# Optimization experiments

Hardware: AMD Instinct MI355X
Metric: run time of the kernel (lower is better)

Reference implementation:

```python
import jax, jax.numpy as jnp
import numpy as np

B, T, D, H, N = 16, 512, 256, 4, 10
DK = D // H
EPS = 1e-12  # espnet LayerNorm eps


def _pe(t, d):
    # espnet PositionalEncoding table
    pos = np.arange(t, dtype=np.float32)[:, None]
    div = np.exp(np.arange(0, d, 2, dtype=np.float32) * (-np.log(10000.0) / d))
    pe = np.zeros((t, d), dtype=np.float32)
    pe[:, 0::2] = np.sin(pos * div)
    pe[:, 1::2] = np.cos(pos * div)
    return jnp.asarray(pe)


def _ln(x, g, b):
    m = jnp.mean(x, -1, keepdims=True)
    v = jnp.var(x, -1, keepdims=True)
    return (x - m) * jax.lax.rsqrt(v + EPS) * g + b


def _forward(x, x_lengths, lids, Wq, bq, Wk, bk, Wv, bv, Wo, bo, W1, b1, W2, b2, g1, be1, g2, be2, gf, bef):
    b, t, d = x.shape
    pe = _pe(t, d)
    pad = jnp.arange(t)[None, :] < x_lengths[:, None]          # [b,t] non-pad mask
    amask = pad[:, None, None, :]                               # [b,1,1,t] key mask
    onehot = (lids[:, None] == jnp.arange(N)[None, :]).astype(x.dtype)  # [b,N]
    h0 = x * np.float32(np.sqrt(d)) + pe[None]                  # scaled input + pos-enc (shared across experts)
    neg = jnp.finfo(x.dtype).min
    out = jnp.zeros_like(x)
    for z in range(N):  # fixed small set of structurally-distinct experts
        # pre-norm self-attention block
        hn = _ln(h0, g1[z], be1[z])
        q = (hn @ Wq[z] + bq[z]).reshape(b, t, H, DK).transpose(0, 2, 1, 3)
        k_ = (hn @ Wk[z] + bk[z]).reshape(b, t, H, DK).transpose(0, 2, 1, 3)
        v_ = (hn @ Wv[z] + bv[z]).reshape(b, t, H, DK).transpose(0, 2, 1, 3)
        scores = jnp.einsum('bhqd,bhkd->bhqk', q, k_) / np.float32(np.sqrt(DK))
        attn = jax.nn.softmax(jnp.where(amask, scores, neg), axis=-1)
        attn = jnp.where(amask, attn, jnp.zeros((), x.dtype))
        ctx = jnp.einsum('bhqk,bhkd->bhqd', attn, v_).transpose(0, 2, 1, 3).reshape(b, t, d)
        h = h0 + ctx @ Wo[z] + bo[z]
        # pre-norm feed-forward block
        hn2 = _ln(h, g2[z], be2[z])
        h = h + jax.nn.relu(hn2 @ W1[z] + b1[z]) @ W2[z] + b2[z]
        # final after_norm, then one-hot masked combine (== emb_lang sum)
        out = out + onehot[:, z, None, None] * _ln(h, gf[z], bef[z])
    return out


def setup_inputs() -> dict:
    key = jax.random.key(0)
    ks = jax.random.split(key, 12)
    s = np.float32(0.02)
    FF = 4 * D
    return {
        'x': jax.random.normal(ks[0], (B, T, D), jnp.float32),
        'x_lengths': jax.random.randint(ks[1], (B,), T // 2, T + 1),
        'lids': jax.random.randint(ks[2], (B,), 0, N),
        'Wq': jax.random.normal(ks[3], (N, D, D), jnp.float32) * s,
        'bq': jnp.zeros((N, D), jnp.float32),
        'Wk': jax.random.normal(ks[4], (N, D, D), jnp.float32) * s,
        'bk': jnp.zeros((N, D), jnp.float32),
        'Wv': jax.random.normal(ks[5], (N, D, D), jnp.float32) * s,
        'bv': jnp.zeros((N, D), jnp.float32),
        'Wo': jax.random.normal(ks[6], (N, D, D), jnp.float32) * s,
        'bo': jnp.zeros((N, D), jnp.float32),
        'W1': jax.random.normal(ks[7], (N, D, FF), jnp.float32) * s,
        'b1': jnp.zeros((N, FF), jnp.float32),
        'W2': jax.random.normal(ks[8], (N, FF, D), jnp.float32) * s,
        'b2': jnp.zeros((N, D), jnp.float32),
        'g1': jnp.ones((N, D), jnp.float32),
        'be1': jnp.zeros((N, D), jnp.float32),
        'g2': jnp.ones((N, D), jnp.float32),
        'be2': jnp.zeros((N, D), jnp.float32),
        'gf': jnp.ones((N, D), jnp.float32),
        'bef': jnp.zeros((N, D), jnp.float32),
    }


def reference(x, x_lengths, lids, Wq, bq, Wk, bk, Wv, bv, Wo, bo, W1, b1, W2, b2, g1, be1, g2, be2, gf, bef):
    return _forward(x, x_lengths, lids, Wq, bq, Wk, bk, Wv, bv, Wo, bo, W1, b1, W2, b2, g1, be1, g2, be2, gf, bef)
```

## Files before the change

kernel.cpp:

```cpp
#include <hip/hip_runtime.h>

typedef unsigned short u16;
typedef __bf16 bf16x8 __attribute__((ext_vector_type(8)));
typedef float  f32x4  __attribute__((ext_vector_type(4)));
typedef unsigned int   u32x4 __attribute__((ext_vector_type(4)));
typedef unsigned short u16x4 __attribute__((ext_vector_type(4)));

#define DEV __device__ __forceinline__

#define NB   16
#define TT   512
#define DD   256
#define HH   4
#define DKH  64
#define NLANG 10
#define FFD  1024

DEV u16 f2bf(float f) {
  unsigned int u = __builtin_bit_cast(unsigned int, f);
  return (u16)((u + 0x7fffu + ((u >> 16) & 1u)) >> 16);
}

DEV float bf2f(u16 u) {
  unsigned int x = ((unsigned int)u) << 16;
  return __builtin_bit_cast(float, x);
}

DEV f32x4 zero4() { f32x4 z; z[0]=0.f; z[1]=0.f; z[2]=0.f; z[3]=0.f; return z; }

typedef __attribute__((address_space(1))) const unsigned int g_as1;
typedef __attribute__((address_space(3))) unsigned int l_as3;
DEV void load_lds16(const void* g, void* l) {
  __builtin_amdgcn_global_load_lds((g_as1*)g, (l_as3*)l, 16, 0, 0);
}

DEV bf16x8 lds_frag(const u16* lds, int row, int slot) {
  return *(const bf16x8*)(lds + row * 64 + ((slot ^ (row & 7)) << 3));
}

__global__ __launch_bounds__(256) void pre_kernel(
    const float* __restrict__ Wq, const float* __restrict__ Wk,
    const float* __restrict__ Wv, const float* __restrict__ Wo,
    const float* __restrict__ W1, const float* __restrict__ W2,
    u16* __restrict__ wtq, u16* __restrict__ wtk, u16* __restrict__ wtv,
    u16* __restrict__ wto, u16* __restrict__ wt1, u16* __restrict__ wt2,
    const float* __restrict__ x, u16* __restrict__ h0, u16* __restrict__ hn,
    const float* __restrict__ g, const float* __restrict__ be,
    const int* __restrict__ lids) {
  __shared__ u16 tile[64][33];
  const int bx = blockIdx.x;
  if (bx < 3840) {
    const float* src; u16* dst; int R, C, z, r0, c0;
    if (bx < 1280) {
      const int w = bx / 320, rem = bx % 320;
      src = (w == 0) ? Wq : (w == 1) ? Wk : (w == 2) ? Wv : Wo;
      dst = (w == 0) ? wtq : (w == 1) ? wtk : (w == 2) ? wtv : wto;
      R = 256; C = 256; z = rem >> 5;
      const int rc = rem & 31; r0 = (rc >> 3) * 64; c0 = (rc & 7) * 32;
    } else if (bx < 2560) {
      const int rem = bx - 1280; src = W1; dst = wt1; R = 256; C = 1024;
      z = rem >> 7; const int rc = rem & 127; r0 = (rc >> 5) * 64; c0 = (rc & 31) * 32;
    } else {
      const int rem = bx - 2560; src = W2; dst = wt2; R = 1024; C = 256;
      z = rem >> 7; const int rc = rem & 127; r0 = (rc >> 3) * 64; c0 = (rc & 7) * 32;
    }
    bool used = false;
#pragma unroll
    for (int i = 0; i < NB; ++i) used |= (lids[i] == z);
    if (!used) return;
    const float* s = src + (size_t)z * R * C;
    u16* d = dst + (size_t)z * R * C;
    const int tx = threadIdx.x & 31, ty = threadIdx.x >> 5;
#pragma unroll
    for (int rr = 0; rr < 8; ++rr) {
      const int r = ty + rr * 8;
      tile[r][tx] = f2bf(s[(size_t)(r0 + r) * C + c0 + tx]);
    }
    __syncthreads();
#pragma unroll
    for (int rr = 0; rr < 4; ++rr) {
      const int cc = ty + rr * 8;
      const unsigned int lo = tile[tx * 2][cc], hi = tile[tx * 2 + 1][cc];
      *(unsigned int*)(d + (size_t)(c0 + cc) * R + r0 + tx * 2) = lo | (hi << 16);
    }
  } else {
    const int wave = threadIdx.x >> 6, lane = threadIdx.x & 63;
    const int row = (bx - 3840) * 4 + wave;
    const int b = row >> 9, t = row & 511;
    const int z = lids[b];
    const int c0 = lane * 4;
    const float4 xv = *(const float4*)(x + (size_t)row * DD + c0);
    const float kPE = -9.21034037197618f / 256.0f;
    float div0 = __expf(kPE * (float)c0);
    float div1 = __expf(kPE * (float)(c0 + 2));
    float a0 = div0 * (float)t, a1 = div1 * (float)t;
    float h[4];
    h[0] = xv.x * 16.0f + sinf(a0);
    h[1] = xv.y * 16.0f + cosf(a0);
    h[2] = xv.z * 16.0f + sinf(a1);
    h[3] = xv.w * 16.0f + cosf(a1);
    float s = h[0] + h[1] + h[2] + h[3];
    float ss = h[0]*h[0] + h[1]*h[1] + h[2]*h[2] + h[3]*h[3];
#pragma unroll
    for (int d = 1; d < 64; d <<= 1) { s += __shfl_xor(s, d); ss += __shfl_xor(ss, d); }
    float mean = s * (1.0f / 256.0f);
    float var  = ss * (1.0f / 256.0f) - mean * mean;
    float rstd = rsqrtf(var + 1e-12f);
    u16x4 h0v;
#pragma unroll
    for (int j = 0; j < 4; ++j) h0v[j] = f2bf(h[j]);
    *(u16x4*)(h0 + (size_t)row * DD + c0) = h0v;
    u16x4 o;
#pragma unroll
    for (int j = 0; j < 4; ++j)
      o[j] = f2bf((h[j] - mean) * rstd * g[z * DD + c0 + j] + be[z * DD + c0 + j]);
    *(u16x4*)(hn + (size_t)row * DD + c0) = o;
  }
}

DEV void gemm_tile(const u16* __restrict__ A, const u16* __restrict__ W, int K,
                   int m0, int n0, u16* Alds, u16* Blds, f32x4 acc[4][4]) {
  const int tid = threadIdx.x;
  const int lane = tid & 63;
  const int wave = tid >> 6;
  const int wm = wave >> 1, wn = wave & 1;
  const int l15 = lane & 15, lhi = lane >> 4;
  const int lr = lane >> 3, lsl = lane & 7;
  const u16* srcA[4]; const u16* srcB[4];
#pragma unroll
  for (int j = 0; j < 4; ++j) {
    const int r = wave * 32 + j * 8 + lr;
    srcA[j] = A + (size_t)(m0 + r) * K + ((lsl ^ (r & 7)) << 3);
    srcB[j] = W + (size_t)(n0 + r) * K + ((lsl ^ (r & 7)) << 3);
  }
  for (int k0 = 0; k0 < K; k0 += 64) {
#pragma unroll
    for (int j = 0; j < 4; ++j) {
      load_lds16(srcA[j] + k0, Alds + (wave * 32 + j * 8) * 64);
      load_lds16(srcB[j] + k0, Blds + (wave * 32 + j * 8) * 64);
    }
    __syncthreads();
#pragma unroll
    for (int ks = 0; ks < 2; ++ks) {
      const int slot = ks * 4 + lhi;
      bf16x8 af[4], bfr[4];
#pragma unroll
      for (int m = 0; m < 4; ++m)
        af[m] = lds_frag(Alds, wm * 64 + m * 16 + l15, slot);
#pragma unroll
      for (int n = 0; n < 4; ++n)
        bfr[n] = lds_frag(Blds, wn * 64 + n * 16 + l15, slot);
#pragma unroll
      for (int m = 0; m < 4; ++m)
#pragma unroll
        for (int n = 0; n < 4; ++n)
          acc[m][n] = __builtin_amdgcn_mfma_f32_16x16x32_bf16(af[m], bfr[n], acc[m][n], 0, 0, 0);
    }
    __syncthreads();
  }
}

template<int EPI>
__global__ __launch_bounds__(256) void gemm_kernel(const u16* __restrict__ A,
                                                   const u16* __restrict__ Wt,
                                                   const float* __restrict__ bias,
                                                   void* __restrict__ outp,
                                                   const int* __restrict__ lids,
                                                   int N, int K) {
  __shared__ u16 Alds[128 * 64];
  __shared__ u16 Blds[128 * 64];
  const int b = blockIdx.z;
  const int z = lids[b];
  const int m0 = blockIdx.y * 128, n0 = blockIdx.x * 128;
  f32x4 acc[4][4];
#pragma unroll
  for (int i = 0; i < 4; ++i)
#pragma unroll
    for (int j = 0; j < 4; ++j) acc[i][j] = zero4();
  gemm_tile(A + (size_t)b * TT * K, Wt + (size_t)z * N * K, K, m0, n0, Alds, Blds, acc);
  const int lane = threadIdx.x & 63, wave = threadIdx.x >> 6;
  const int wm = wave >> 1, wn = wave & 1;
  const int l15 = lane & 15, lhi = lane >> 4;
  float bvv[4];
#pragma unroll
  for (int n = 0; n < 4; ++n) bvv[n] = bias[(size_t)z * N + n0 + wn * 64 + n * 16 + l15];
#pragma unroll
  for (int m = 0; m < 4; ++m) {
    const int grow = m0 + wm * 64 + m * 16 + lhi * 4;
#pragma unroll
    for (int n = 0; n < 4; ++n) {
      const int gcol = n0 + wn * 64 + n * 16 + l15;
#pragma unroll
      for (int r = 0; r < 4; ++r) {
        float v = acc[m][n][r] + bvv[n];
        size_t idx = (size_t)b * TT * N + (size_t)(grow + r) * N + gcol;
        if (EPI == 1) ((u16*)outp)[idx] = f2bf(v > 0.f ? v : 0.f);
        else ((u16*)outp)[idx] = f2bf(v);
      }
    }
  }
}

__global__ __launch_bounds__(256) void gemm_qkv(const u16* __restrict__ A,
                                                const u16* __restrict__ wtq,
                                                const u16* __restrict__ wtk,
                                                const u16* __restrict__ wtv,
                                                const float* __restrict__ bq,
                                                const float* __restrict__ bk,
                                                const float* __restrict__ bv,
                                                u16* __restrict__ qo,
                                                u16* __restrict__ ko,
                                                u16* __restrict__ vto,
                                                const int* __restrict__ lids) {
  __shared__ u16 Alds[128 * 64];
  __shared__ u16 Blds[128 * 64];
  const int b = blockIdx.z & 15, which = blockIdx.z >> 4;
  const int z = lids[b];
  const u16* W = (which == 0) ? wtq : (which == 1) ? wtk : wtv;
  const float* bias = (which == 0) ? bq : (which == 1) ? bk : bv;
  const int m0 = blockIdx.y * 128, n0 = blockIdx.x * 128;
  f32x4 acc[4][4];
#pragma unroll
  for (int i = 0; i < 4; ++i)
#pragma unroll
    for (int j = 0; j < 4; ++j) acc[i][j] = zero4();
  gemm_tile(A + (size_t)b * TT * DD, W + (size_t)z * DD * DD, DD, m0, n0, Alds, Blds, acc);
  const int lane = threadIdx.x & 63, wave = threadIdx.x >> 6;
  const int wm = wave >> 1, wn = wave & 1;
  const int l15 = lane & 15, lhi = lane >> 4;
  float bvv[4];
#pragma unroll
  for (int n = 0; n < 4; ++n) bvv[n] = bias[(size_t)z * DD + n0 + wn * 64 + n * 16 + l15];
  if (which < 2) {
    u16* out = (which == 0) ? qo : ko;
#pragma unroll
    for (int m = 0; m < 4; ++m) {
      const int grow = m0 + wm * 64 + m * 16 + lhi * 4;
#pragma unroll
      for (int n = 0; n < 4; ++n) {
        const int gcol = n0 + wn * 64 + n * 16 + l15;
#pragma unroll
        for (int r = 0; r < 4; ++r)
          out[(size_t)b * TT * DD + (size_t)(grow + r) * DD + gcol] = f2bf(acc[m][n][r] + bvv[n]);
      }
    }
  } else {
#pragma unroll
    for (int m = 0; m < 4; ++m) {
      const int grow = m0 + wm * 64 + m * 16 + lhi * 4;
#pragma unroll
      for (int n = 0; n < 4; ++n) {
        const int gcol = n0 + wn * 64 + n * 16 + l15;
        u16x4 pk;
#pragma unroll
        for (int r = 0; r < 4; ++r) pk[r] = f2bf(acc[m][n][r] + bvv[n]);
        *(u16x4*)(vto + (size_t)(b * HH + (gcol >> 6)) * DKH * TT + (size_t)(gcol & 63) * TT + grow) = pk;
      }
    }
  }
}

__global__ __launch_bounds__(256, 1) void attn_fused(const u16* __restrict__ q,
                                                     const u16* __restrict__ k,
                                                     const u16* __restrict__ vt,
                                                     u16* __restrict__ ctx,
                                                     const int* __restrict__ lens) {
  __shared__ u16 Klds[128 * 64];
  __shared__ u16 Vlds[64 * 128];
  __shared__ u16 Plds[128 * 128];
  __shared__ float Lred[2][128];
  const int qt = blockIdx.x, bh = blockIdx.y;
  const int b = bh >> 2, h = bh & 3;
  const int len = lens[b];
  const int nt = (len + 127) >> 7;
  const int tid = threadIdx.x, lane = tid & 63, wave = tid >> 6;
  const int wm = wave >> 1, wn = wave & 1;
  const int l15 = lane & 15, lhi = lane >> 4;
  const int lr = lane >> 3, lsl = lane & 7;
  const int m0 = qt * 128;
  const u16* qb = q + (size_t)b * TT * DD + h * DKH;
  const u16* kb = k + (size_t)b * TT * DD + h * DKH;
  const u16* vtb = vt + (size_t)bh * DKH * TT;
  const float SC = 0.125f * 1.4426950408889634f;

  bf16x8 qf[4][2];
#pragma unroll
  for (int m = 0; m < 4; ++m)
#pragma unroll
    for (int ks = 0; ks < 2; ++ks)
      qf[m][ks] = *(const bf16x8*)(qb + (size_t)(m0 + wm * 64 + m * 16 + l15) * DD + ks * 32 + lhi * 8);

  ((float*)Lred)[tid] = 0.f;

  f32x4 oacc[2][4];
#pragma unroll
  for (int i = 0; i < 2; ++i)
#pragma unroll
    for (int j = 0; j < 4; ++j) oacc[i][j] = zero4();

  for (int kt = 0; kt < nt; ++kt) {
#pragma unroll
    for (int j = 0; j < 4; ++j) {
      const int r = wave * 32 + j * 8 + lr;
      load_lds16(kb + (size_t)(kt * 128 + r) * DD + ((lsl ^ (r & 7)) << 3),
                 Klds + (wave * 32 + j * 8) * 64);
    }
#pragma unroll
    for (int j = 0; j < 4; ++j) {
      const int rv = wave * 16 + j * 4 + (lane >> 4);
      const int cc = lane & 15;
      load_lds16(vtb + (size_t)rv * TT + kt * 128 + ((cc ^ (rv & 7)) << 3),
                 Vlds + (wave * 16 + j * 4) * 128);
    }
    __syncthreads();
    f32x4 sacc[4][4];
#pragma unroll
    for (int i = 0; i < 4; ++i)
#pragma unroll
      for (int j = 0; j < 4; ++j) sacc[i][j] = zero4();
#pragma unroll
    for (int ks = 0; ks < 2; ++ks) {
      const int slot = ks * 4 + lhi;
      bf16x8 bfr[4];
#pragma unroll
      for (int n = 0; n < 4; ++n)
        bfr[n] = lds_frag(Klds, wn * 64 + n * 16 + l15, slot);
#pragma unroll
      for (int m = 0; m < 4; ++m)
#pragma unroll
        for (int n = 0; n < 4; ++n)
          sacc[m][n] = __builtin_amdgcn_mfma_f32_16x16x32_bf16(qf[m][ks], bfr[n], sacc[m][n], 0, 0, 0);
    }
    float lsum[4][4];
#pragma unroll
    for (int m = 0; m < 4; ++m)
#pragma unroll
      for (int r = 0; r < 4; ++r) lsum[m][r] = 0.f;
#pragma unroll
    for (int m = 0; m < 4; ++m) {
#pragma unroll
      for (int n = 0; n < 4; ++n) {
        const int col = wn * 64 + n * 16 + l15;
        const bool in = (kt * 128 + col) < len;
#pragma unroll
        for (int r = 0; r < 4; ++r) {
          const int row = wm * 64 + m * 16 + lhi * 4 + r;
          float p = exp2f(sacc[m][n][r] * SC);
          p = in ? p : 0.f;
          lsum[m][r] += p;
          Plds[row * 128 + (col ^ ((row & 7) << 3))] = (u16)(__builtin_bit_cast(unsigned int, p) >> 16);
        }
      }
    }
#pragma unroll
    for (int d = 1; d < 16; d <<= 1)
#pragma unroll
      for (int m = 0; m < 4; ++m)
#pragma unroll
        for (int r = 0; r < 4; ++r) lsum[m][r] += __shfl_xor(lsum[m][r], d);
    if (l15 == 0) {
#pragma unroll
      for (int m = 0; m < 4; ++m)
#pragma unroll
        for (int r = 0; r < 4; ++r)
          Lred[wn][wm * 64 + m * 16 + lhi * 4 + r] += lsum[m][r];
    }
    __syncthreads();
#pragma unroll
    for (int ks = 0; ks < 4; ++ks) {
      const int cb = ks * 32 + lhi * 8;
      bf16x8 af[2], bfr[4];
#pragma unroll
      for (int mm = 0; mm < 2; ++mm) {
        const int row = wave * 32 + mm * 16 + l15;
        af[mm] = *(const bf16x8*)(Plds + row * 128 + (cb ^ ((row & 7) << 3)));
      }
#pragma unroll
      for (int n = 0; n < 4; ++n) {
        const int row = n * 16 + l15;
        bfr[n] = *(const bf16x8*)(Vlds + row * 128 + (cb ^ ((row & 7) << 3)));
      }
#pragma unroll
      for (int mm = 0; mm < 2; ++mm)
#pragma unroll
        for (int n = 0; n < 4; ++n)
          oacc[mm][n] = __builtin_amdgcn_mfma_f32_16x16x32_bf16(af[mm], bfr[n], oacc[mm][n], 0, 0, 0);
    }
    __syncthreads();
  }

  u16* cb2 = ctx + (size_t)b * TT * DD + h * DKH;
#pragma unroll
  for (int mm = 0; mm < 2; ++mm) {
#pragma unroll
    for (int r = 0; r < 4; ++r) {
      const int row = wave * 32 + mm * 16 + lhi * 4 + r;
      const float linv = 1.0f / (Lred[0][row] + Lred[1][row]);
#pragma unroll
      for (int n = 0; n < 4; ++n)
        cb2[(size_t)(m0 + row) * DD + n * 16 + l15] = f2bf(oacc[mm][n][r] * linv);
    }
  }
}

template<int FINAL>
__global__ __launch_bounds__(512) void gemm_ln_kernel(
    const u16* __restrict__ A, const u16* __restrict__ Wt,
    const float* __restrict__ bias, const u16* __restrict__ res,
    void* __restrict__ outf, u16* __restrict__ outbf,
    const float* __restrict__ g, const float* __restrict__ be,
    const int* __restrict__ lids, int K) {
  __shared__ u16 Alds[32 * 64];
  __shared__ u16 Blds[256 * 64];
  __shared__ float Sred[2][4][16];
  __shared__ float SSred[2][4][16];
  const int b = blockIdx.y;
  const int z = lids[b];
  const int m0 = blockIdx.x * 32;
  const int tid = threadIdx.x, lane = tid & 63, wave = tid >> 6;
  const int l15 = lane & 15, lhi = lane >> 4;
  const int lr = lane >> 3, lsl = lane & 7;
  const u16* Ab = A + (size_t)b * TT * K;
  const u16* Wb = Wt + (size_t)z * 256 * K;
  const u16* srcA = Ab;
  if (wave < 4) {
    const int rA = wave * 8 + lr;
    srcA = Ab + (size_t)(m0 + rA) * K + ((lsl ^ (rA & 7)) << 3);
  }
  const u16* srcB[4];
#pragma unroll
  for (int j = 0; j < 4; ++j) {
    const int rB = wave * 32 + j * 8 + lr;
    srcB[j] = Wb + (size_t)rB * K + ((lsl ^ (rB & 7)) << 3);
  }
  f32x4 acc[4];
#pragma unroll
  for (int n = 0; n < 4; ++n) acc[n] = zero4();
  for (int k0 = 0; k0 < K; k0 += 64) {
    if (wave < 4) load_lds16(srcA + k0, Alds + (wave * 8) * 64);
#pragma unroll
    for (int j = 0; j < 4; ++j)
      load_lds16(srcB[j] + k0, Blds + (wave * 32 + j * 8) * 64);
    __syncthreads();
#pragma unroll
    for (int ks = 0; ks < 2; ++ks) {
      const int slot = ks * 4 + lhi;
      bf16x8 af = lds_frag(Alds, (wave >> 2) * 16 + l15, slot);
#pragma unroll
      for (int n = 0; n < 4; ++n) {
        bf16x8 bf = lds_frag(Blds, (wave & 3) * 64 + n * 16 + l15, slot);
        acc[n] = __builtin_amdgcn_mfma_f32_16x16x32_bf16(af, bf, acc[n], 0, 0, 0);
      }
    }
    __syncthreads();
  }
  const int rbase = m0 + (wave >> 2) * 16;
  const int cq = (wave & 3) * 64;
  float bv[4], gv[4], bev[4];
#pragma unroll
  for (int n = 0; n < 4; ++n) {
    const int col = cq + n * 16 + l15;
    bv[n]  = bias[(size_t)z * 256 + col];
    gv[n]  = g[(size_t)z * 256 + col];
    bev[n] = be[(size_t)z * 256 + col];
  }
  float v[4][4];
  float sr[4] = {0.f, 0.f, 0.f, 0.f}, ssr[4] = {0.f, 0.f, 0.f, 0.f};
#pragma unroll
  for (int n = 0; n < 4; ++n) {
#pragma unroll
    for (int r = 0; r < 4; ++r) {
      const size_t idx = ((size_t)b * TT + rbase + lhi * 4 + r) * 256 + cq + n * 16 + l15;
      float t = acc[n][r] + bv[n] + bf2f(res[idx]);
      v[n][r] = t;
      sr[r] += t;
      ssr[r] += t * t;
    }
  }
#pragma unroll
  for (int d = 1; d < 16; d <<= 1)
#pragma unroll
    for (int r = 0; r < 4; ++r) { sr[r] += __shfl_xor(sr[r], d); ssr[r] += __shfl_xor(ssr[r], d); }
  if (l15 == 0) {
#pragma unroll
    for (int r = 0; r < 4; ++r) {
      Sred[wave >> 2][wave & 3][lhi * 4 + r] = sr[r];
      SSred[wave >> 2][wave & 3][lhi * 4 + r] = ssr[r];
    }
  }
  __syncthreads();
#pragma unroll
  for (int r = 0; r < 4; ++r) {
    float tot = 0.f, tss = 0.f;
#pragma unroll
    for (int qd = 0; qd < 4; ++qd) {
      tot += Sred[wave >> 2][qd][lhi * 4 + r];
      tss += SSred[wave >> 2][qd][lhi * 4 + r];
    }
    const float mean = tot * (1.0f / 256.0f);
    const float var  = tss * (1.0f / 256.0f) - mean * mean;
    const float rstd = rsqrtf(var + 1e-12f);
#pragma unroll
    for (int n = 0; n < 4; ++n) {
      const size_t idx = ((size_t)b * TT + rbase + lhi * 4 + r) * 256 + cq + n * 16 + l15;
      const float ln = (v[n][r] - mean) * rstd * gv[n] + bev[n];
      if (FINAL) {
        ((float*)outf)[idx] = ln;
      } else {
        ((u16*)outf)[idx] = f2bf(v[n][r]);
        outbf[idx] = f2bf(ln);
      }
    }
  }
}

extern "C" void kernel_launch(void* const* d_in, const int* in_sizes, int n_in,
                              void* d_out, int out_size, void* d_ws, size_t ws_size,
                              hipStream_t stream) {
  (void)in_sizes; (void)n_in; (void)out_size; (void)ws_size;
  const float* x    = (const float*)d_in[0];
  const int*   xlen = (const int*)d_in[1];
  const int*   lids = (const int*)d_in[2];
  const float* Wq = (const float*)d_in[3];
  const float* bq = (const float*)d_in[4];
  const float* Wk = (const float*)d_in[5];
  const float* bk = (const float*)d_in[6];
  const float* Wv = (const float*)d_in[7];
  const float* bv = (const float*)d_in[8];
  const float* Wo = (const float*)d_in[9];
  const float* bo = (const float*)d_in[10];
  const float* W1 = (const float*)d_in[11];
  const float* b1 = (const float*)d_in[12];
  const float* W2 = (const float*)d_in[13];
  const float* b2 = (const float*)d_in[14];
  const float* g1 = (const float*)d_in[15];
  const float* be1= (const float*)d_in[16];
  const float* g2 = (const float*)d_in[17];
  const float* be2= (const float*)d_in[18];
  const float* gf = (const float*)d_in[19];
  const float* bef= (const float*)d_in[20];

  char* ws = (char*)d_ws;
  size_t off = 0;
  auto alloc = [&](size_t bytes) -> void* {
    void* p = ws + off;
    off = (off + bytes + 255) & ~(size_t)255;
    return p;
  };
  u16* wtq = (u16*)alloc((size_t)NLANG * DD * DD * 2);
  u16* wtk = (u16*)alloc((size_t)NLANG * DD * DD * 2);
  u16* wtv = (u16*)alloc((size_t)NLANG * DD * DD * 2);
  u16* wto = (u16*)alloc((size_t)NLANG * DD * DD * 2);
  u16* wt1 = (u16*)alloc((size_t)NLANG * DD * FFD * 2);
  u16* wt2 = (u16*)alloc((size_t)NLANG * FFD * DD * 2);
  u16* h0  = (u16*)alloc((size_t)NB * TT * DD * 2);
  u16* hc  = (u16*)alloc((size_t)NB * TT * DD * 2);
  u16* hn  = (u16*)alloc((size_t)NB * TT * DD * 2);
  u16* qb  = (u16*)alloc((size_t)NB * TT * DD * 2);
  u16* kb  = (u16*)alloc((size_t)NB * TT * DD * 2);
  u16* vtb = (u16*)alloc((size_t)NB * TT * DD * 2);
  u16* ctx = (u16*)alloc((size_t)NB * TT * DD * 2);
  u16* ffn = (u16*)alloc((size_t)NB * TT * FFD * 2);

  pre_kernel<<<dim3(3840 + 2048), 256, 0, stream>>>(
      Wq, Wk, Wv, Wo, W1, W2, wtq, wtk, wtv, wto, wt1, wt2,
      x, h0, hn, g1, be1, lids);

  gemm_qkv<<<dim3(2, 4, 48), 256, 0, stream>>>(hn, wtq, wtk, wtv, bq, bk, bv, qb, kb, vtb, lids);

  attn_fused<<<dim3(4, 64), 256, 0, stream>>>(qb, kb, vtb, ctx, xlen);

  gemm_ln_kernel<0><<<dim3(16, NB), 512, 0, stream>>>(ctx, wto, bo, h0, hc, hn, g2, be2, lids, DD);

  gemm_kernel<1><<<dim3(8, 4, NB), 256, 0, stream>>>(hn, wt1, b1, ffn, lids, FFD, DD);

  gemm_ln_kernel<1><<<dim3(16, NB), 512, 0, stream>>>(ffn, wt2, b2, hc, (float*)d_out, nullptr, gf, bef, lids, FFD);
}
```

Baseline: 85.21 us.

## Fuse all stages into one cooperative persistent kernel with grid syncs

```diff
diff --git a/kernel.cpp b/kernel.cpp
--- a/kernel.cpp
+++ b/kernel.cpp
@@ -1,4 +1,6 @@
 #include <hip/hip_runtime.h>
+#include <hip/hip_cooperative_groups.h>
+namespace cg = cooperative_groups;
 
 typedef unsigned short u16;
 typedef __bf16 bf16x8 __attribute__((ext_vector_type(8)));
@@ -38,91 +40,10 @@
   return *(const bf16x8*)(lds + row * 64 + ((slot ^ (row & 7)) << 3));
 }
 
-__global__ __launch_bounds__(256) void pre_kernel(
-    const float* __restrict__ Wq, const float* __restrict__ Wk,
-    const float* __restrict__ Wv, const float* __restrict__ Wo,
-    const float* __restrict__ W1, const float* __restrict__ W2,
-    u16* __restrict__ wtq, u16* __restrict__ wtk, u16* __restrict__ wtv,
-    u16* __restrict__ wto, u16* __restrict__ wt1, u16* __restrict__ wt2,
-    const float* __restrict__ x, u16* __restrict__ h0, u16* __restrict__ hn,
-    const float* __restrict__ g, const float* __restrict__ be,
-    const int* __restrict__ lids) {
-  __shared__ u16 tile[64][33];
-  const int bx = blockIdx.x;
-  if (bx < 3840) {
-    const float* src; u16* dst; int R, C, z, r0, c0;
-    if (bx < 1280) {
-      const int w = bx / 320, rem = bx % 320;
-      src = (w == 0) ? Wq : (w == 1) ? Wk : (w == 2) ? Wv : Wo;
-      dst = (w == 0) ? wtq : (w == 1) ? wtk : (w == 2) ? wtv : wto;
-      R = 256; C = 256; z = rem >> 5;
-      const int rc = rem & 31; r0 = (rc >> 3) * 64; c0 = (rc & 7) * 32;
-    } else if (bx < 2560) {
-      const int rem = bx - 1280; src = W1; dst = wt1; R = 256; C = 1024;
-      z = rem >> 7; const int rc = rem & 127; r0 = (rc >> 5) * 64; c0 = (rc & 31) * 32;
-    } else {
-      const int rem = bx - 2560; src = W2; dst = wt2; R = 1024; C = 256;
-      z = rem >> 7; const int rc = rem & 127; r0 = (rc >> 3) * 64; c0 = (rc & 7) * 32;
-    }
-    bool used = false;
-#pragma unroll
-    for (int i = 0; i < NB; ++i) used |= (lids[i] == z);
-    if (!used) return;
-    const float* s = src + (size_t)z * R * C;
-    u16* d = dst + (size_t)z * R * C;
-    const int tx = threadIdx.x & 31, ty = threadIdx.x >> 5;
-#pragma unroll
-    for (int rr = 0; rr < 8; ++rr) {
-      const int r = ty + rr * 8;
-      tile[r][tx] = f2bf(s[(size_t)(r0 + r) * C + c0 + tx]);
-    }
-    __syncthreads();
-#pragma unroll
-    for (int rr = 0; rr < 4; ++rr) {
-      const int cc = ty + rr * 8;
-      const unsigned int lo = tile[tx * 2][cc], hi = tile[tx * 2 + 1][cc];
-      *(unsigned int*)(d + (size_t)(c0 + cc) * R + r0 + tx * 2) = lo | (hi << 16);
-    }
-  } else {
-    const int wave = threadIdx.x >> 6, lane = threadIdx.x & 63;
-    const int row = (bx - 3840) * 4 + wave;
-    const int b = row >> 9, t = row & 511;
-    const int z = lids[b];
-    const int c0 = lane * 4;
-    const float4 xv = *(const float4*)(x + (size_t)row * DD + c0);
-    const float kPE = -9.21034037197618f / 256.0f;
-    float div0 = __expf(kPE * (float)c0);
-    float div1 = __expf(kPE * (float)(c0 + 2));
-    float a0 = div0 * (float)t, a1 = div1 * (float)t;
-    float h[4];
-    h[0] = xv.x * 16.0f + sinf(a0);
-    h[1] = xv.y * 16.0f + cosf(a0);
-    h[2] = xv.z * 16.0f + sinf(a1);
-    h[3] = xv.w * 16.0f + cosf(a1);
-    float s = h[0] + h[1] + h[2] + h[3];
-    float ss = h[0]*h[0] + h[1]*h[1] + h[2]*h[2] + h[3]*h[3];
-#pragma unroll
-    for (int d = 1; d < 64; d <<= 1) { s += __shfl_xor(s, d); ss += __shfl_xor(ss, d); }
-    float mean = s * (1.0f / 256.0f);
-    float var  = ss * (1.0f / 256.0f) - mean * mean;
-    float rstd = rsqrtf(var + 1e-12f);
-    u16x4 h0v;
-#pragma unroll
-    for (int j = 0; j < 4; ++j) h0v[j] = f2bf(h[j]);
-    *(u16x4*)(h0 + (size_t)row * DD + c0) = h0v;
-    u16x4 o;
-#pragma unroll
-    for (int j = 0; j < 4; ++j)
-      o[j] = f2bf((h[j] - mean) * rstd * g[z * DD + c0 + j] + be[z * DD + c0 + j]);
-    *(u16x4*)(hn + (size_t)row * DD + c0) = o;
-  }
-}
-
-DEV void gemm_tile(const u16* __restrict__ A, const u16* __restrict__ W, int K,
-                   int m0, int n0, u16* Alds, u16* Blds, f32x4 acc[4][4]) {
-  const int tid = threadIdx.x;
-  const int lane = tid & 63;
-  const int wave = tid >> 6;
+DEV void gemm128(const u16* __restrict__ A, const u16* __restrict__ W, int K,
+                 int m0, int n0, u16* Alds, u16* Blds, f32x4 acc[4][4],
+                 bool valid, int tid) {
+  const int lane = tid & 63, wave = tid >> 6;
   const int wm = wave >> 1, wn = wave & 1;
   const int l15 = lane & 15, lhi = lane >> 4;
   const int lr = lane >> 3, lsl = lane & 7;
@@ -134,10 +55,12 @@
     srcB[j] = W + (size_t)(n0 + r) * K + ((lsl ^ (r & 7)) << 3);
   }
   for (int k0 = 0; k0 < K; k0 += 64) {
-#pragma unroll
-    for (int j = 0; j < 4; ++j) {
-      load_lds16(srcA[j] + k0, Alds + (wave * 32 + j * 8) * 64);
-      load_lds16(srcB[j] + k0, Blds + (wave * 32 + j * 8) * 64);
+    if (valid) {
+#pragma unroll
+      for (int j = 0; j < 4; ++j) {
+        load_lds16(srcA[j] + k0, Alds + (wave * 32 + j * 8) * 64);
+        load_lds16(srcB[j] + k0, Blds + (wave * 32 + j * 8) * 64);
+      }
     }
     __syncthreads();
 #pragma unroll
@@ -160,264 +83,19 @@
   }
 }
 
-template<int EPI>
-__global__ __launch_bounds__(256) void gemm_kernel(const u16* __restrict__ A,
-                                                   const u16* __restrict__ Wt,
-                                                   const float* __restrict__ bias,
-                                                   void* __restrict__ outp,
-                                                   const int* __restrict__ lids,
-                                                   int N, int K) {
-  __shared__ u16 Alds[128 * 64];
-  __shared__ u16 Blds[128 * 64];
-  const int b = blockIdx.z;
+DEV void gemm_ln_stage(const u16* __restrict__ A, const u16* __restrict__ Wt,
+                       const float* __restrict__ bias, const u16* __restrict__ res,
+                       void* outf, u16* outbf, const float* __restrict__ g,
+                       const float* __restrict__ be, const int* __restrict__ lids,
+                       int K, int bx, char* smem, int tid512, bool FINAL) {
+  u16* Alds = (u16*)smem;
+  u16* Blds = (u16*)(smem + 4096);
+  float* Sred = (float*)(smem + 36864);
+  float* SSred = Sred + 128;
+  const int b = bx >> 4;
   const int z = lids[b];
-  const int m0 = blockIdx.y * 128, n0 = blockIdx.x * 128;
-  f32x4 acc[4][4];
-#pragma unroll
-  for (int i = 0; i < 4; ++i)
-#pragma unroll
-    for (int j = 0; j < 4; ++j) acc[i][j] = zero4();
-  gemm_tile(A + (size_t)b * TT * K, Wt + (size_t)z * N * K, K, m0, n0, Alds, Blds, acc);
-  const int lane = threadIdx.x & 63, wave = threadIdx.x >> 6;
-  const int wm = wave >> 1, wn = wave & 1;
-  const int l15 = lane & 15, lhi = lane >> 4;
-  float bvv[4];
-#pragma unroll
-  for (int n = 0; n < 4; ++n) bvv[n] = bias[(size_t)z * N + n0 + wn * 64 + n * 16 + l15];
-#pragma unroll
-  for (int m = 0; m < 4; ++m) {
-    const int grow = m0 + wm * 64 + m * 16 + lhi * 4;
-#pragma unroll
-    for (int n = 0; n < 4; ++n) {
-      const int gcol = n0 + wn * 64 + n * 16 + l15;
-#pragma unroll
-      for (int r = 0; r < 4; ++r) {
-        float v = acc[m][n][r] + bvv[n];
-        size_t idx = (size_t)b * TT * N + (size_t)(grow + r) * N + gcol;
-        if (EPI == 1) ((u16*)outp)[idx] = f2bf(v > 0.f ? v : 0.f);
-        else ((u16*)outp)[idx] = f2bf(v);
-      }
-    }
-  }
-}
-
-__global__ __launch_bounds__(256) void gemm_qkv(const u16* __restrict__ A,
-                                                const u16* __restrict__ wtq,
-                                                const u16* __restrict__ wtk,
-                                                const u16* __restrict__ wtv,
-                                                const float* __restrict__ bq,
-                                                const float* __restrict__ bk,
-                                                const float* __restrict__ bv,
-                                                u16* __restrict__ qo,
-                                                u16* __restrict__ ko,
-                                                u16* __restrict__ vto,
-                                                const int* __restrict__ lids) {
-  __shared__ u16 Alds[128 * 64];
-  __shared__ u16 Blds[128 * 64];
-  const int b = blockIdx.z & 15, which = blockIdx.z >> 4;
-  const int z = lids[b];
-  const u16* W = (which == 0) ? wtq : (which == 1) ? wtk : wtv;
-  const float* bias = (which == 0) ? bq : (which == 1) ? bk : bv;
-  const int m0 = blockIdx.y * 128, n0 = blockIdx.x * 128;
-  f32x4 acc[4][4];
-#pragma unroll
-  for (int i = 0; i < 4; ++i)
-#pragma unroll
-    for (int j = 0; j < 4; ++j) acc[i][j] = zero4();
-  gemm_tile(A + (size_t)b * TT * DD, W + (size_t)z * DD * DD, DD, m0, n0, Alds, Blds, acc);
-  const int lane = threadIdx.x & 63, wave = threadIdx.x >> 6;
-  const int wm = wave >> 1, wn = wave & 1;
-  const int l15 = lane & 15, lhi = lane >> 4;
-  float bvv[4];
-#pragma unroll
-  for (int n = 0; n < 4; ++n) bvv[n] = bias[(size_t)z * DD + n0 + wn * 64 + n * 16 + l15];
-  if (which < 2) {
-    u16* out = (which == 0) ? qo : ko;
-#pragma unroll
-    for (int m = 0; m < 4; ++m) {
-      const int grow = m0 + wm * 64 + m * 16 + lhi * 4;
-#pragma unroll
-      for (int n = 0; n < 4; ++n) {
-        const int gcol = n0 + wn * 64 + n * 16 + l15;
-#pragma unroll
-        for (int r = 0; r < 4; ++r)
-          out[(size_t)b * TT * DD + (size_t)(grow + r) * DD + gcol] = f2bf(acc[m][n][r] + bvv[n]);
-      }
-    }
-  } else {
-#pragma unroll
-    for (int m = 0; m < 4; ++m) {
-      const int grow = m0 + wm * 64 + m * 16 + lhi * 4;
-#pragma unroll
-      for (int n = 0; n < 4; ++n) {
-        const int gcol = n0 + wn * 64 + n * 16 + l15;
-        u16x4 pk;
-#pragma unroll
-        for (int r = 0; r < 4; ++r) pk[r] = f2bf(acc[m][n][r] + bvv[n]);
-        *(u16x4*)(vto + (size_t)(b * HH + (gcol >> 6)) * DKH * TT + (size_t)(gcol & 63) * TT + grow) = pk;
-      }
-    }
-  }
-}
-
-__global__ __launch_bounds__(256, 1) void attn_fused(const u16* __restrict__ q,
-                                                     const u16* __restrict__ k,
-                                                     const u16* __restrict__ vt,
-                                                     u16* __restrict__ ctx,
-                                                     const int* __restrict__ lens) {
-  __shared__ u16 Klds[128 * 64];
-  __shared__ u16 Vlds[64 * 128];
-  __shared__ u16 Plds[128 * 128];
-  __shared__ float Lred[2][128];
-  const int qt = blockIdx.x, bh = blockIdx.y;
-  const int b = bh >> 2, h = bh & 3;
-  const int len = lens[b];
-  const int nt = (len + 127) >> 7;
-  const int tid = threadIdx.x, lane = tid & 63, wave = tid >> 6;
-  const int wm = wave >> 1, wn = wave & 1;
-  const int l15 = lane & 15, lhi = lane >> 4;
-  const int lr = lane >> 3, lsl = lane & 7;
-  const int m0 = qt * 128;
-  const u16* qb = q + (size_t)b * TT * DD + h * DKH;
-  const u16* kb = k + (size_t)b * TT * DD + h * DKH;
-  const u16* vtb = vt + (size_t)bh * DKH * TT;
-  const float SC = 0.125f * 1.4426950408889634f;
-
-  bf16x8 qf[4][2];
-#pragma unroll
-  for (int m = 0; m < 4; ++m)
-#pragma unroll
-    for (int ks = 0; ks < 2; ++ks)
-      qf[m][ks] = *(const bf16x8*)(qb + (size_t)(m0 + wm * 64 + m * 16 + l15) * DD + ks * 32 + lhi * 8);
-
-  ((float*)Lred)[tid] = 0.f;
-
-  f32x4 oacc[2][4];
-#pragma unroll
-  for (int i = 0; i < 2; ++i)
-#pragma unroll
-    for (int j = 0; j < 4; ++j) oacc[i][j] = zero4();
-
-  for (int kt = 0; kt < nt; ++kt) {
-#pragma unroll
-    for (int j = 0; j < 4; ++j) {
-      const int r = wave * 32 + j * 8 + lr;
-      load_lds16(kb + (size_t)(kt * 128 + r) * DD + ((lsl ^ (r & 7)) << 3),
-                 Klds + (wave * 32 + j * 8) * 64);
-    }
-#pragma unroll
-    for (int j = 0; j < 4; ++j) {
-      const int rv = wave * 16 + j * 4 + (lane >> 4);
-      const int cc = lane & 15;
-      load_lds16(vtb + (size_t)rv * TT + kt * 128 + ((cc ^ (rv & 7)) << 3),
-                 Vlds + (wave * 16 + j * 4) * 128);
-    }
-    __syncthreads();
-    f32x4 sacc[4][4];
-#pragma unroll
-    for (int i = 0; i < 4; ++i)
-#pragma unroll
-      for (int j = 0; j < 4; ++j) sacc[i][j] = zero4();
-#pragma unroll
-    for (int ks = 0; ks < 2; ++ks) {
-      const int slot = ks * 4 + lhi;
-      bf16x8 bfr[4];
-#pragma unroll
-      for (int n = 0; n < 4; ++n)
-        bfr[n] = lds_frag(Klds, wn * 64 + n * 16 + l15, slot);
-#pragma unroll
-      for (int m = 0; m < 4; ++m)
-#pragma unroll
-        for (int n = 0; n < 4; ++n)
-          sacc[m][n] = __builtin_amdgcn_mfma_f32_16x16x32_bf16(qf[m][ks], bfr[n], sacc[m][n], 0, 0, 0);
-    }
-    float lsum[4][4];
-#pragma unroll
-    for (int m = 0; m < 4; ++m)
-#pragma unroll
-      for (int r = 0; r < 4; ++r) lsum[m][r] = 0.f;
-#pragma unroll
-    for (int m = 0; m < 4; ++m) {
-#pragma unroll
-      for (int n = 0; n < 4; ++n) {
-        const int col = wn * 64 + n * 16 + l15;
-        const bool in = (kt * 128 + col) < len;
-#pragma unroll
-        for (int r = 0; r < 4; ++r) {
-          const int row = wm * 64 + m * 16 + lhi * 4 + r;
-          float p = exp2f(sacc[m][n][r] * SC);
-          p = in ? p : 0.f;
-          lsum[m][r] += p;
-          Plds[row * 128 + (col ^ ((row & 7) << 3))] = (u16)(__builtin_bit_cast(unsigned int, p) >> 16);
-        }
-      }
-    }
-#pragma unroll
-    for (int d = 1; d < 16; d <<= 1)
-#pragma unroll
-      for (int m = 0; m < 4; ++m)
-#pragma unroll
-        for (int r = 0; r < 4; ++r) lsum[m][r] += __shfl_xor(lsum[m][r], d);
-    if (l15 == 0) {
-#pragma unroll
-      for (int m = 0; m < 4; ++m)
-#pragma unroll
-        for (int r = 0; r < 4; ++r)
-          Lred[wn][wm * 64 + m * 16 + lhi * 4 + r] += lsum[m][r];
-    }
-    __syncthreads();
-#pragma unroll
-    for (int ks = 0; ks < 4; ++ks) {
-      const int cb = ks * 32 + lhi * 8;
-      bf16x8 af[2], bfr[4];
-#pragma unroll
-      for (int mm = 0; mm < 2; ++mm) {
-        const int row = wave * 32 + mm * 16 + l15;
-        af[mm] = *(const bf16x8*)(Plds + row * 128 + (cb ^ ((row & 7) << 3)));
-      }
-#pragma unroll
-      for (int n = 0; n < 4; ++n) {
-        const int row = n * 16 + l15;
-        bfr[n] = *(const bf16x8*)(Vlds + row * 128 + (cb ^ ((row & 7) << 3)));
-      }
-#pragma unroll
-      for (int mm = 0; mm < 2; ++mm)
-#pragma unroll
-        for (int n = 0; n < 4; ++n)
-          oacc[mm][n] = __builtin_amdgcn_mfma_f32_16x16x32_bf16(af[mm], bfr[n], oacc[mm][n], 0, 0, 0);
-    }
-    __syncthreads();
-  }
-
-  u16* cb2 = ctx + (size_t)b * TT * DD + h * DKH;
-#pragma unroll
-  for (int mm = 0; mm < 2; ++mm) {
-#pragma unroll
-    for (int r = 0; r < 4; ++r) {
-      const int row = wave * 32 + mm * 16 + lhi * 4 + r;
-      const float linv = 1.0f / (Lred[0][row] + Lred[1][row]);
-#pragma unroll
-      for (int n = 0; n < 4; ++n)
-        cb2[(size_t)(m0 + row) * DD + n * 16 + l15] = f2bf(oacc[mm][n][r] * linv);
-    }
-  }
-}
-
-template<int FINAL>
-__global__ __launch_bounds__(512) void gemm_ln_kernel(
-    const u16* __restrict__ A, const u16* __restrict__ Wt,
-    const float* __restrict__ bias, const u16* __restrict__ res,
-    void* __restrict__ outf, u16* __restrict__ outbf,
-    const float* __restrict__ g, const float* __restrict__ be,
-    const int* __restrict__ lids, int K) {
-  __shared__ u16 Alds[32 * 64];
-  __shared__ u16 Blds[256 * 64];
-  __shared__ float Sred[2][4][16];
-  __shared__ float SSred[2][4][16];
-  const int b = blockIdx.y;
-  const int z = lids[b];
-  const int m0 = blockIdx.x * 32;
-  const int tid = threadIdx.x, lane = tid & 63, wave = tid >> 6;
+  const int m0 = (bx & 15) * 32;
+  const int lane = tid512 & 63, wave = tid512 >> 6;
   const int l15 = lane & 15, lhi = lane >> 4;
   const int lr = lane >> 3, lsl = lane & 7;
   const u16* Ab = A + (size_t)b * TT * K;
@@ -484,8 +162,9 @@
   if (l15 == 0) {
 #pragma unroll
     for (int r = 0; r < 4; ++r) {
-      Sred[wave >> 2][wave & 3][lhi * 4 + r] = sr[r];
-      SSred[wave >> 2][wave & 3][lhi * 4 + r] = ssr[r];
+      const int si = ((wave >> 2) * 4 + (wave & 3)) * 16 + lhi * 4 + r;
+      Sred[si] = sr[r];
+      SSred[si] = ssr[r];
     }
   }
   __syncthreads();
@@ -494,8 +173,9 @@
     float tot = 0.f, tss = 0.f;
 #pragma unroll
     for (int qd = 0; qd < 4; ++qd) {
-      tot += Sred[wave >> 2][qd][lhi * 4 + r];
-      tss += SSred[wave >> 2][qd][lhi * 4 + r];
+      const int si = ((wave >> 2) * 4 + qd) * 16 + lhi * 4 + r;
+      tot += Sred[si];
+      tss += SSred[si];
     }
     const float mean = tot * (1.0f / 256.0f);
     const float var  = tss * (1.0f / 256.0f) - mean * mean;
@@ -512,6 +192,360 @@
       }
     }
   }
+  __syncthreads();
+}
+
+__global__ __launch_bounds__(512, 2) void mega_kernel(
+    const float* __restrict__ x, const int* __restrict__ xlen, const int* __restrict__ lids,
+    const float* __restrict__ Wq, const float* __restrict__ bq,
+    const float* __restrict__ Wk, const float* __restrict__ bk,
+    const float* __restrict__ Wv, const float* __restrict__ bv,
+    const float* __restrict__ Wo, const float* __restrict__ bo,
+    const float* __restrict__ W1, const float* __restrict__ b1,
+    const float* __restrict__ W2, const float* __restrict__ b2,
+    const float* __restrict__ g1, const float* __restrict__ be1,
+    const float* __restrict__ g2, const float* __restrict__ be2,
+    const float* __restrict__ gf, const float* __restrict__ bef,
+    u16* wtq, u16* wtk, u16* wtv, u16* wto, u16* wt1, u16* wt2,
+    u16* h0, u16* hc, u16* hn, u16* qb, u16* kb, u16* vtb, u16* ctx, u16* ffn,
+    float* out) {
+  __shared__ char smem[69632];
+  cg::grid_group grid = cg::this_grid();
+  const int tid512 = threadIdx.x;
+  const int sub = tid512 >> 8;
+  const int tid = tid512 & 255;
+  const int bx = blockIdx.x;
+
+  {
+    u16 (*tile)[33] = (u16 (*)[33])(smem + sub * (64 * 33 * 2));
+    for (int it = 0; it < 12; ++it) {
+      const int unit = it * 512 + bx * 2 + sub;
+      const bool isT = unit < 3840;
+      const bool isE = !isT && unit < 5888;
+      const float* src = nullptr; u16* dst = nullptr;
+      int R = 256, C = 256, z = 0, r0 = 0, c0 = 0;
+      bool used = false;
+      if (isT) {
+        if (unit < 1280) {
+          const int w = unit / 320, rem = unit % 320;
+          src = (w == 0) ? Wq : (w == 1) ? Wk : (w == 2) ? Wv : Wo;
+          dst = (w == 0) ? wtq : (w == 1) ? wtk : (w == 2) ? wtv : wto;
+          R = 256; C = 256; z = rem >> 5;
+          const int rc = rem & 31; r0 = (rc >> 3) * 64; c0 = (rc & 7) * 32;
+        } else if (unit < 2560) {
+          const int rem = unit - 1280; src = W1; dst = wt1; R = 256; C = 1024;
+          z = rem >> 7; const int rc = rem & 127; r0 = (rc >> 5) * 64; c0 = (rc & 31) * 32;
+        } else {
+          const int rem = unit - 2560; src = W2; dst = wt2; R = 1024; C = 256;
+          z = rem >> 7; const int rc = rem & 127; r0 = (rc >> 3) * 64; c0 = (rc & 7) * 32;
+        }
+#pragma unroll
+        for (int i = 0; i < NB; ++i) used |= (lids[i] == z);
+      }
+      const int tx = tid & 31, ty = tid >> 5;
+      if (isT && used) {
+        const float* s = src + (size_t)z * R * C;
+#pragma unroll
+        for (int rr = 0; rr < 8; ++rr) {
+          const int r = ty + rr * 8;
+          tile[r][tx] = f2bf(s[(size_t)(r0 + r) * C + c0 + tx]);
+        }
+      }
+      __syncthreads();
+      if (isT && used) {
+        u16* d = dst + (size_t)z * R * C;
+#pragma unroll
+        for (int rr = 0; rr < 4; ++rr) {
+          const int cc = ty + rr * 8;
+          const unsigned int lo = tile[tx * 2][cc], hi = tile[tx * 2 + 1][cc];
+          *(unsigned int*)(d + (size_t)(c0 + cc) * R + r0 + tx * 2) = lo | (hi << 16);
+        }
+      }
+      if (isE) {
+        const int wave = tid >> 6, lane = tid & 63;
+        const int row = (unit - 3840) * 4 + wave;
+        const int b = row >> 9, t = row & 511;
+        const int z2 = lids[b];
+        const int c0e = lane * 4;
+        const float4 xv = *(const float4*)(x + (size_t)row * DD + c0e);
+        const float kPE = -9.21034037197618f / 256.0f;
+        float div0 = __expf(kPE * (float)c0e);
+        float div1 = __expf(kPE * (float)(c0e + 2));
+        float a0 = div0 * (float)t, a1 = div1 * (float)t;
+        float h[4];
+        h[0] = xv.x * 16.0f + __sinf(a0);
+        h[1] = xv.y * 16.0f + __cosf(a0);
+        h[2] = xv.z * 16.0f + __sinf(a1);
+        h[3] = xv.w * 16.0f + __cosf(a1);
+        float s = h[0] + h[1] + h[2] + h[3];
+        float ss = h[0]*h[0] + h[1]*h[1] + h[2]*h[2] + h[3]*h[3];
+#pragma unroll
+        for (int d = 1; d < 64; d <<= 1) { s += __shfl_xor(s, d); ss += __shfl_xor(ss, d); }
+        float mean = s * (1.0f / 256.0f);
+        float var  = ss * (1.0f / 256.0f) - mean * mean;
+        float rstd = rsqrtf(var + 1e-12f);
+        u16x4 h0v;
+#pragma unroll
+        for (int j = 0; j < 4; ++j) h0v[j] = f2bf(h[j]);
+        *(u16x4*)(h0 + (size_t)row * DD + c0e) = h0v;
+        u16x4 o;
+#pragma unroll
+        for (int j = 0; j < 4; ++j)
+          o[j] = f2bf((h[j] - mean) * rstd * g1[z2 * DD + c0e + j] + be1[z2 * DD + c0e + j]);
+        *(u16x4*)(hn + (size_t)row * DD + c0e) = o;
+      }
+      __syncthreads();
+    }
+  }
+  grid.sync();
+
+  {
+    const int unit = bx * 2 + sub;
+    const bool valid = unit < 384;
+    u16* Alds = (u16*)(smem + sub * 32768);
+    u16* Blds = Alds + 128 * 64;
+    const int nx = unit & 1, my = (unit >> 1) & 3, bz = unit >> 3;
+    const int b = bz & 15, which = (bz >> 4) & 3;
+    const int z = lids[b];
+    const u16* W = (which == 0) ? wtq : (which == 1) ? wtk : wtv;
+    const float* bias = (which == 0) ? bq : (which == 1) ? bk : bv;
+    const int m0 = my * 128, n0 = nx * 128;
+    f32x4 acc[4][4];
+#pragma unroll
+    for (int i = 0; i < 4; ++i)
+#pragma unroll
+      for (int j = 0; j < 4; ++j) acc[i][j] = zero4();
+    gemm128(hn + (size_t)b * TT * DD, W + (size_t)z * DD * DD, DD, m0, n0,
+            Alds, Blds, acc, valid, tid);
+    if (valid) {
+      const int lane = tid & 63, wave = tid >> 6;
+      const int wm = wave >> 1, wn = wave & 1;
+      const int l15 = lane & 15, lhi = lane >> 4;
+      float bvv[4];
+#pragma unroll
+      for (int n = 0; n < 4; ++n) bvv[n] = bias[(size_t)z * DD + n0 + wn * 64 + n * 16 + l15];
+      if (which < 2) {
+        u16* outp = (which == 0) ? qb : kb;
+#pragma unroll
+        for (int m = 0; m < 4; ++m) {
+          const int grow = m0 + wm * 64 + m * 16 + lhi * 4;
+#pragma unroll
+          for (int n = 0; n < 4; ++n) {
+            const int gcol = n0 + wn * 64 + n * 16 + l15;
+#pragma unroll
+            for (int r = 0; r < 4; ++r)
+              outp[(size_t)b * TT * DD + (size_t)(grow + r) * DD + gcol] = f2bf(acc[m][n][r] + bvv[n]);
+          }
+        }
+      } else {
+#pragma unroll
+        for (int m = 0; m < 4; ++m) {
+          const int grow = m0 + wm * 64 + m * 16 + lhi * 4;
+#pragma unroll
+          for (int n = 0; n < 4; ++n) {
+            const int gcol = n0 + wn * 64 + n * 16 + l15;
+            u16x4 pk;
+#pragma unroll
+            for (int r = 0; r < 4; ++r) pk[r] = f2bf(acc[m][n][r] + bvv[n]);
+            *(u16x4*)(vtb + (size_t)(b * HH + (gcol >> 6)) * DKH * TT + (size_t)(gcol & 63) * TT + grow) = pk;
+          }
+        }
+      }
+    }
+  }
+  grid.sync();
+
+  {
+    const int unit = bx;
+    const int qt = unit & 3, bh = unit >> 2;
+    const int b = bh >> 2, h = bh & 3;
+    u16* Klds = (u16*)smem;
+    u16* Vlds = Klds + 128 * 64;
+    u16* Plds = Vlds + 64 * 128;
+    float* Lred = (float*)(Plds + 128 * 128);
+    const bool act0 = (sub == 0);
+    const int len = xlen[b];
+    const int nt = (len + 127) >> 7;
+    const int lane = tid & 63, wave = tid >> 6;
+    const int wm = wave >> 1, wn = wave & 1;
+    const int l15 = lane & 15, lhi = lane >> 4;
+    const int lr = lane >> 3, lsl = lane & 7;
+    const int m0 = qt * 128;
+    const u16* qbp = qb + (size_t)b * TT * DD + h * DKH;
+    const u16* kbp = kb + (size_t)b * TT * DD + h * DKH;
+    const u16* vtp = vtb + (size_t)bh * DKH * TT;
+    const float SC = 0.125f * 1.4426950408889634f;
+
+    bf16x8 qf[4][2];
+    if (act0) {
+#pragma unroll
+      for (int m = 0; m < 4; ++m)
+#pragma unroll
+        for (int ks = 0; ks < 2; ++ks)
+          qf[m][ks] = *(const bf16x8*)(qbp + (size_t)(m0 + wm * 64 + m * 16 + l15) * DD + ks * 32 + lhi * 8);
+    }
+    if (tid512 < 256) ((float*)Lred)[tid512] = 0.f;
+
+    f32x4 oacc[2][4];
+#pragma unroll
+    for (int i = 0; i < 2; ++i)
+#pragma unroll
+      for (int j = 0; j < 4; ++j) oacc[i][j] = zero4();
+
+    for (int kt = 0; kt < 4; ++kt) {
+      const bool active = act0 && (kt < nt);
+      if (active) {
+#pragma unroll
+        for (int j = 0; j < 4; ++j) {
+          const int r = wave * 32 + j * 8 + lr;
+          load_lds16(kbp + (size_t)(kt * 128 + r) * DD + ((lsl ^ (r & 7)) << 3),
+                     Klds + (wave * 32 + j * 8) * 64);
+        }
+#pragma unroll
+        for (int j = 0; j < 4; ++j) {
+          const int rv = wave * 16 + j * 4 + (lane >> 4);
+          const int cc = lane & 15;
+          load_lds16(vtp + (size_t)rv * TT + kt * 128 + ((cc ^ (rv & 7)) << 3),
+                     Vlds + (wave * 16 + j * 4) * 128);
+        }
+      }
+      __syncthreads();
+      if (active) {
+        f32x4 sacc[4][4];
+#pragma unroll
+        for (int i = 0; i < 4; ++i)
+#pragma unroll
+          for (int j = 0; j < 4; ++j) sacc[i][j] = zero4();
+#pragma unroll
+        for (int ks = 0; ks < 2; ++ks) {
+          const int slot = ks * 4 + lhi;
+          bf16x8 bfr[4];
+#pragma unroll
+          for (int n = 0; n < 4; ++n)
+            bfr[n] = lds_frag(Klds, wn * 64 + n * 16 + l15, slot);
+#pragma unroll
+          for (int m = 0; m < 4; ++m)
+#pragma unroll
+            for (int n = 0; n < 4; ++n)
+              sacc[m][n] = __builtin_amdgcn_mfma_f32_16x16x32_bf16(qf[m][ks], bfr[n], sacc[m][n], 0, 0, 0);
+        }
+        float lsum[4][4];
+#pragma unroll
+        for (int m = 0; m < 4; ++m)
+#pragma unroll
+          for (int r = 0; r < 4; ++r) lsum[m][r] = 0.f;
+#pragma unroll
+        for (int m = 0; m < 4; ++m) {
+#pragma unroll
+          for (int n = 0; n < 4; ++n) {
+            const int col = wn * 64 + n * 16 + l15;
+            const bool in = (kt * 128 + col) < len;
+#pragma unroll
+            for (int r = 0; r < 4; ++r) {
+              const int row = wm * 64 + m * 16 + lhi * 4 + r;
+              float p = exp2f(sacc[m][n][r] * SC);
+              p = in ? p : 0.f;
+              lsum[m][r] += p;
+              Plds[row * 128 + (col ^ ((row & 7) << 3))] = (u16)(__builtin_bit_cast(unsigned int, p) >> 16);
+            }
+          }
+        }
+#pragma unroll
+        for (int d = 1; d < 16; d <<= 1)
+#pragma unroll
+          for (int m = 0; m < 4; ++m)
+#pragma unroll
+            for (int r = 0; r < 4; ++r) lsum[m][r] += __shfl_xor(lsum[m][r], d);
+        if (l15 == 0) {
+#pragma unroll
+          for (int m = 0; m < 4; ++m)
+#pragma unroll
+            for (int r = 0; r < 4; ++r)
+              Lred[wn * 128 + wm * 64 + m * 16 + lhi * 4 + r] += lsum[m][r];
+        }
+      }
+      __syncthreads();
+      if (active) {
+#pragma unroll
+        for (int ks = 0; ks < 4; ++ks) {
+          const int cb = ks * 32 + lhi * 8;
+          bf16x8 af[2], bfr[4];
+#pragma unroll
+          for (int mm = 0; mm < 2; ++mm) {
+            const int row = wave * 32 + mm * 16 + l15;
+            af[mm] = *(const bf16x8*)(Plds + row * 128 + (cb ^ ((row & 7) << 3)));
+          }
+#pragma unroll
+          for (int n = 0; n < 4; ++n) {
+            const int row = n * 16 + l15;
+            bfr[n] = *(const bf16x8*)(Vlds + row * 128 + (cb ^ ((row & 7) << 3)));
+          }
+#pragma unroll
+          for (int mm = 0; mm < 2; ++mm)
+#pragma unroll
+            for (int n = 0; n < 4; ++n)
+              oacc[mm][n] = __builtin_amdgcn_mfma_f32_16x16x32_bf16(af[mm], bfr[n], oacc[mm][n], 0, 0, 0);
+        }
+      }
+      __syncthreads();
+    }
+    if (act0) {
+      u16* cb2 = ctx + (size_t)b * TT * DD + h * DKH;
+#pragma unroll
+      for (int mm = 0; mm < 2; ++mm) {
+#pragma unroll
+        for (int r = 0; r < 4; ++r) {
+          const int row = wave * 32 + mm * 16 + lhi * 4 + r;
+          const float linv = 1.0f / (Lred[row] + Lred[128 + row]);
+#pragma unroll
+          for (int n = 0; n < 4; ++n)
+            cb2[(size_t)(m0 + row) * DD + n * 16 + l15] = f2bf(oacc[mm][n][r] * linv);
+        }
+      }
+    }
+  }
+  grid.sync();
+
+  gemm_ln_stage(ctx, wto, bo, h0, hc, hn, g2, be2, lids, DD, bx, smem, tid512, false);
+  grid.sync();
+
+  {
+    const int unit = bx * 2 + sub;
+    u16* Alds = (u16*)(smem + sub * 32768);
+    u16* Blds = Alds + 128 * 64;
+    const int nx = unit & 7, my = (unit >> 3) & 3, b = unit >> 5;
+    const int z = lids[b];
+    const int m0 = my * 128, n0 = nx * 128;
+    f32x4 acc[4][4];
+#pragma unroll
+    for (int i = 0; i < 4; ++i)
+#pragma unroll
+      for (int j = 0; j < 4; ++j) acc[i][j] = zero4();
+    gemm128(hn + (size_t)b * TT * DD, wt1 + (size_t)z * FFD * DD, DD, m0, n0,
+            Alds, Blds, acc, true, tid);
+    const int lane = tid & 63, wave = tid >> 6;
+    const int wm = wave >> 1, wn = wave & 1;
+    const int l15 = lane & 15, lhi = lane >> 4;
+    float bvv[4];
+#pragma unroll
+    for (int n = 0; n < 4; ++n) bvv[n] = b1[(size_t)z * FFD + n0 + wn * 64 + n * 16 + l15];
+#pragma unroll
+    for (int m = 0; m < 4; ++m) {
+      const int grow = m0 + wm * 64 + m * 16 + lhi * 4;
+#pragma unroll
+      for (int n = 0; n < 4; ++n) {
+        const int gcol = n0 + wn * 64 + n * 16 + l15;
+#pragma unroll
+        for (int r = 0; r < 4; ++r) {
+          float v = acc[m][n][r] + bvv[n];
+          ffn[(size_t)b * TT * FFD + (size_t)(grow + r) * FFD + gcol] = f2bf(v > 0.f ? v : 0.f);
+        }
+      }
+    }
+  }
+  grid.sync();
+
+  gemm_ln_stage(ffn, wt2, b2, hc, out, nullptr, gf, bef, lids, FFD, bx, smem, tid512, true);
 }
 
 extern "C" void kernel_launch(void* const* d_in, const int* in_sizes, int n_in,
@@ -561,18 +595,19 @@
   u16* vtb = (u16*)alloc((size_t)NB * TT * DD * 2);
   u16* ctx = (u16*)alloc((size_t)NB * TT * DD * 2);
   u16* ffn = (u16*)alloc((size_t)NB * TT * FFD * 2);
-
-  pre_kernel<<<dim3(3840 + 2048), 256, 0, stream>>>(
-      Wq, Wk, Wv, Wo, W1, W2, wtq, wtk, wtv, wto, wt1, wt2,
-      x, h0, hn, g1, be1, lids);
-
-  gemm_qkv<<<dim3(2, 4, 48), 256, 0, stream>>>(hn, wtq, wtk, wtv, bq, bk, bv, qb, kb, vtb, lids);
-
-  attn_fused<<<dim3(4, 64), 256, 0, stream>>>(qb, kb, vtb, ctx, xlen);
-
-  gemm_ln_kernel<0><<<dim3(16, NB), 512, 0, stream>>>(ctx, wto, bo, h0, hc, hn, g2, be2, lids, DD);
-
-  gemm_kernel<1><<<dim3(8, 4, NB), 256, 0, stream>>>(hn, wt1, b1, ffn, lids, FFD, DD);
-
-  gemm_ln_kernel<1><<<dim3(16, NB), 512, 0, stream>>>(ffn, wt2, b2, hc, (float*)d_out, nullptr, gf, bef, lids, FFD);
-}
+  float* outp = (float*)d_out;
+
+  void* args[] = {
+    (void*)&x, (void*)&xlen, (void*)&lids,
+    (void*)&Wq, (void*)&bq, (void*)&Wk, (void*)&bk,
+    (void*)&Wv, (void*)&bv, (void*)&Wo, (void*)&bo,
+    (void*)&W1, (void*)&b1, (void*)&W2, (void*)&b2,
+    (void*)&g1, (void*)&be1, (void*)&g2, (void*)&be2,
+    (void*)&gf, (void*)&bef,
+    (void*)&wtq, (void*)&wtk, (void*)&wtv, (void*)&wto, (void*)&wt1, (void*)&wt2,
+    (void*)&h0, (void*)&hc, (void*)&hn, (void*)&qb, (void*)&kb, (void*)&vtb,
+    (void*)&ctx, (void*)&ffn, (void*)&outp
+  };
+  hipLaunchCooperativeKernel((const void*)mega_kernel, dim3(256), dim3(512),
+                             args, 0, stream);
+}
```

Measured after the change: 285.5 us. 235% more time.
